# Kernel optimization log

Hardware: AMD Instinct MI355X
Metric: run time of the kernel (lower is better)

Reference implementation:

```python
import jax, jax.numpy as jnp
import numpy as np

K = 32        # top-k per row (init kwarg k)
TAU = 1.0     # gumbel temperature (init kwarg tau)
EPS = 1e-08
NEG_INF = -1e9


def setup_inputs() -> dict:
    key = jax.random.key(0)
    k1, k2 = jax.random.split(key)
    N = 8192
    logits = jax.random.normal(k1, (N, N), dtype=jnp.float32)
    u = jax.random.uniform(k2, (N, N), dtype=jnp.float32)
    return {"logits": logits, "u": u}


def reference(logits, u):
    # Gumbel noise: -log(-log(U + eps) + eps), matching torch.rand_like usage
    gumbel = -jnp.log(-jnp.log(u + EPS) + EPS)
    perturbed = (logits + gumbel) / TAU
    # Row-wise top-k indices on perturbed logits
    _, top_idx = jax.lax.top_k(perturbed, K)          # [N, K]
    # Scatter a hard 0/1 mask at the selected indices
    N = logits.shape[0]
    rows = jnp.arange(N)[:, None]                      # [N, 1]
    mask = jnp.zeros_like(logits).at[rows, top_idx].set(1.0)
    # Masked softmax over the ORIGINAL logits (noise only selects)
    masked_logits = logits * mask + (1.0 - mask) * NEG_INF
    adjacency = jax.nn.softmax(masked_logits, axis=-1)
    return adjacency
```

## Files before the change

### kernel.cpp

```cpp
#include <hip/hip_runtime.h>
#include <cstdint>

#define ROW_N 8192
#define TPB   256
#define CAP   512

__device__ __forceinline__ unsigned int fkey(float p) {
  unsigned int b = __float_as_uint(p);
  return (b & 0x80000000u) ? ~b : (b | 0x80000000u);
}
__device__ __forceinline__ float fkey_inv(unsigned int t) {
  unsigned int b = (t & 0x80000000u) ? (t & 0x7fffffffu) : ~t;
  return __uint_as_float(b);
}

__device__ __forceinline__ unsigned int akey(float lg, float uu) {
  float l2u = __log2f(uu + 1e-8f);
  float w   = fmaf(l2u, -0.6931471805599453f, 1e-8f);
  float p2  = fmaf(lg, 1.4426950408889634f, -__log2f(w));
  p2 = (w < 1e-5f) ? 3.0e38f : p2;
  return fkey(p2);
}

__device__ __forceinline__ uint64_t shfl_xor_u64(uint64_t v, int m) {
  unsigned int lo = (unsigned int)v, hi = (unsigned int)(v >> 32);
  lo = __shfl_xor(lo, m, 64);
  hi = __shfl_xor(hi, m, 64);
  return ((uint64_t)hi << 32) | lo;
}
__device__ __forceinline__ uint64_t wave_max_u64(uint64_t v) {
#pragma unroll
  for (int s = 32; s >= 1; s >>= 1) {
    uint64_t o = shfl_xor_u64(v, s);
    v = (o > v) ? o : v;
  }
  return v;
}

__global__ __launch_bounds__(TPB) void gumbel_topk_kernel(
    const float* __restrict__ logits, const float* __restrict__ u,
    float* __restrict__ out) {
  const int row  = blockIdx.x;
  const int tid  = threadIdx.x;
  const int lane = tid & 63;
  const int wave = tid >> 6;

  __shared__ unsigned int s_cnt, s_t;
  __shared__ unsigned int s_tmax[TPB];
  __shared__ unsigned int s_idx[CAP];
  __shared__ uint64_t     s_comp[CAP];
  __shared__ float        s_lg[CAP];
  __shared__ float        s_red[8];

  if (tid == 0) { s_cnt = 0; s_t = 0xFFFFFFFFu; }

  const float4* L4 = reinterpret_cast<const float4*>(logits) + (size_t)row * (ROW_N / 4);
  const float4* U4 = reinterpret_cast<const float4*>(u)      + (size_t)row * (ROW_N / 4);
  float4*       O4 = reinterpret_cast<float4*>(out)          + (size_t)row * (ROW_N / 4);

  unsigned int k[32];
  unsigned int M = 0;
#pragma unroll
  for (int j = 0; j < 8; ++j) {
    float4 lv = L4[j * TPB + tid];
    float4 uv = U4[j * TPB + tid];
    k[j * 4 + 0] = akey(lv.x, uv.x);
    k[j * 4 + 1] = akey(lv.y, uv.y);
    k[j * 4 + 2] = akey(lv.z, uv.z);
    k[j * 4 + 3] = akey(lv.w, uv.w);
    M = max(M, max(max(k[j * 4 + 0], k[j * 4 + 1]), max(k[j * 4 + 2], k[j * 4 + 3])));
  }

  {
    float4 z = make_float4(0.f, 0.f, 0.f, 0.f);
#pragma unroll
    for (int j = 0; j < 8; ++j) O4[j * TPB + tid] = z;
  }

  s_tmax[tid] = M;
  __syncthreads();
  {
    unsigned int cnt = 0;
    const uint4* tm4 = reinterpret_cast<const uint4*>(s_tmax);
#pragma unroll 4
    for (int i = 0; i < TPB / 4; ++i) {
      uint4 v = tm4[i];
      cnt += (v.x > M) + (v.y > M) + (v.z > M) + (v.w > M);
    }
    if (cnt < 32) atomicMin(&s_t, M);
  }
  __syncthreads();
  const unsigned int tm = fkey(fkey_inv(s_t) - 0.25f);

#pragma unroll
  for (int j = 0; j < 8; ++j) {
#pragma unroll
    for (int c = 0; c < 4; ++c) {
      if (k[j * 4 + c] >= tm) {
        unsigned int slot = atomicAdd(&s_cnt, 1u);
        if (slot < CAP)
          s_idx[slot] = (unsigned int)(j * TPB + tid) * 4u + (unsigned int)c;
      }
    }
  }
  __syncthreads();
  unsigned int C = s_cnt;

  if (C > CAP) {
#pragma unroll 1
    for (int it = 0; it < 32; ++it) {
      uint64_t lm = 0;
#pragma unroll
      for (int i = 0; i < 32; ++i) {
        unsigned int idx = (unsigned int)((i >> 2) * TPB + tid) * 4u + (unsigned int)(i & 3);
        uint64_t comp = ((uint64_t)k[i] << 13) | (uint64_t)(8191u - idx);
        if (k[i] != 0u && comp > lm) lm = comp;
      }
      uint64_t wm = wave_max_u64(lm);
      if (lm == wm) {
#pragma unroll
        for (int i = 0; i < 32; ++i) {
          unsigned int idx = (unsigned int)((i >> 2) * TPB + tid) * 4u + (unsigned int)(i & 3);
          uint64_t comp = ((uint64_t)k[i] << 13) | (uint64_t)(8191u - idx);
          if (comp == wm) k[i] = 0u;
        }
      }
      if (lane == 0) s_idx[wave * 32 + it] = 8191u - (unsigned int)(wm & 8191u);
    }
    __syncthreads();
    C = 128;
  }

  const float* Lrow = logits + (size_t)row * ROW_N;
  const float* Urow = u      + (size_t)row * ROW_N;
#pragma unroll 1
  for (unsigned int vi = tid; vi < C; vi += TPB) {
    unsigned int idx = s_idx[vi];
    float lg = Lrow[idx];
    float uu = Urow[idx];
    float p  = lg - logf(-logf(uu + 1e-8f) + 1e-8f);
    s_comp[vi] = ((uint64_t)fkey(p) << 13) | (uint64_t)(8191u - idx);
    s_lg[vi]   = lg;
  }
  __syncthreads();

  float m_local = -3.4e38f;
  unsigned int sel = 0;
  float lgs[2];
  unsigned int ids[2];
#pragma unroll
  for (int s = 0; s < 2; ++s) {
    unsigned int vi = tid + s * TPB;
    lgs[s] = 0.f; ids[s] = 0;
    if (vi < C) {
      uint64_t mine = s_comp[vi];
      unsigned int cnt = 0;
#pragma unroll 1
      for (unsigned int i = 0; i < C; ++i) cnt += (s_comp[i] > mine) ? 1u : 0u;
      if (cnt < 32) {
        sel |= (1u << s);
        lgs[s] = s_lg[vi];
        ids[s] = s_idx[vi];
        m_local = fmaxf(m_local, lgs[s]);
      }
    }
  }

  float m = m_local;
#pragma unroll
  for (int s = 32; s >= 1; s >>= 1) m = fmaxf(m, __shfl_xor(m, s, 64));
  if (lane == 0) s_red[wave] = m;
  __syncthreads();
  m = fmaxf(fmaxf(s_red[0], s_red[1]), fmaxf(s_red[2], s_red[3]));

  float e0 = (sel & 1u) ? expf(lgs[0] - m) : 0.f;
  float e1 = (sel & 2u) ? expf(lgs[1] - m) : 0.f;
  float sum = e0 + e1;
#pragma unroll
  for (int s = 32; s >= 1; s >>= 1) sum += __shfl_xor(sum, s, 64);
  if (lane == 0) s_red[4 + wave] = sum;
  __syncthreads();
  sum = (s_red[4] + s_red[5]) + (s_red[6] + s_red[7]);

  float* Orow = out + (size_t)row * ROW_N;
  if (sel & 1u) Orow[ids[0]] = e0 / sum;
  if (sel & 2u) Orow[ids[1]] = e1 / sum;
}

extern "C" void kernel_launch(void* const* d_in, const int* in_sizes, int n_in,
                              void* d_out, int out_size, void* d_ws, size_t ws_size,
                              hipStream_t stream) {
  const float* logits = (const float*)d_in[0];
  const float* u      = (const float*)d_in[1];
  float*       out    = (float*)d_out;
  int rows = in_sizes[0] / ROW_N;
  gumbel_topk_kernel<<<dim3(rows), dim3(TPB), 0, stream>>>(logits, u, out);
}
```

Baseline: 618.2 us.

## Use 1024-thread blocks with wave-level second-max threshold and saturated-key handling

Raises the block size from 256 to 1024 threads, so each thread holds 8 keys instead of 32. The per-thread count over a shared max array is replaced by two wave max reductions that find each wave's second-largest thread max; the minimum across 16 waves becomes the candidate threshold. Saturated Gumbel values now get a lower-bound key and are always admitted as candidates instead of being forced to infinity. This lowers register pressure and the serial work per thread, in exchange for more waves per block, more candidates in the final pairwise ranking, and extra sync cost.

```diff
diff --git a/kernel.cpp b/kernel.cpp
--- a/kernel.cpp
+++ b/kernel.cpp
@@ -2,8 +2,10 @@
 #include <cstdint>
 
 #define ROW_N 8192
-#define TPB   256
-#define CAP   512
+#define TPB   1024
+#define NW    16
+#define EPT   8
+#define CAP   1024
 
 __device__ __forceinline__ unsigned int fkey(float p) {
   unsigned int b = __float_as_uint(p);
@@ -14,12 +16,13 @@
   return __uint_as_float(b);
 }
 
-__device__ __forceinline__ unsigned int akey(float lg, float uu) {
+__device__ __forceinline__ unsigned int akey(float lg, float uu, bool& sat) {
   float l2u = __log2f(uu + 1e-8f);
   float w   = fmaf(l2u, -0.6931471805599453f, 1e-8f);
+  sat = (w < 1e-5f);
   float p2  = fmaf(lg, 1.4426950408889634f, -__log2f(w));
-  p2 = (w < 1e-5f) ? 3.0e38f : p2;
-  return fkey(p2);
+  float lb  = (lg + 11.512925f) * 1.4426950408889634f;
+  return fkey(sat ? lb : p2);
 }
 
 __device__ __forceinline__ uint64_t shfl_xor_u64(uint64_t v, int m) {
@@ -36,8 +39,16 @@
   }
   return v;
 }
+__device__ __forceinline__ unsigned int wave_max_u32(unsigned int v) {
+#pragma unroll
+  for (int s = 32; s >= 1; s >>= 1) {
+    unsigned int o = __shfl_xor(v, s, 64);
+    v = max(v, o);
+  }
+  return v;
+}
 
-__global__ __launch_bounds__(TPB) void gumbel_topk_kernel(
+__global__ __launch_bounds__(TPB, 8) void gumbel_topk_kernel(
     const float* __restrict__ logits, const float* __restrict__ u,
     float* __restrict__ out) {
   const int row  = blockIdx.x;
@@ -45,62 +56,58 @@
   const int lane = tid & 63;
   const int wave = tid >> 6;
 
-  __shared__ unsigned int s_cnt, s_t;
-  __shared__ unsigned int s_tmax[TPB];
+  __shared__ unsigned int s_cnt;
+  __shared__ unsigned int s_tw[NW];
   __shared__ unsigned int s_idx[CAP];
   __shared__ uint64_t     s_comp[CAP];
   __shared__ float        s_lg[CAP];
-  __shared__ float        s_red[8];
+  __shared__ float        s_red[NW];
+  __shared__ float        s_red2[NW];
 
-  if (tid == 0) { s_cnt = 0; s_t = 0xFFFFFFFFu; }
+  if (tid == 0) s_cnt = 0;
 
   const float4* L4 = reinterpret_cast<const float4*>(logits) + (size_t)row * (ROW_N / 4);
   const float4* U4 = reinterpret_cast<const float4*>(u)      + (size_t)row * (ROW_N / 4);
   float4*       O4 = reinterpret_cast<float4*>(out)          + (size_t)row * (ROW_N / 4);
 
-  unsigned int k[32];
+  unsigned int k[EPT];
+  unsigned int satm = 0;
   unsigned int M = 0;
 #pragma unroll
-  for (int j = 0; j < 8; ++j) {
+  for (int j = 0; j < EPT / 4; ++j) {
     float4 lv = L4[j * TPB + tid];
     float4 uv = U4[j * TPB + tid];
-    k[j * 4 + 0] = akey(lv.x, uv.x);
-    k[j * 4 + 1] = akey(lv.y, uv.y);
-    k[j * 4 + 2] = akey(lv.z, uv.z);
-    k[j * 4 + 3] = akey(lv.w, uv.w);
+    bool s0, s1, s2, s3;
+    k[j * 4 + 0] = akey(lv.x, uv.x, s0);
+    k[j * 4 + 1] = akey(lv.y, uv.y, s1);
+    k[j * 4 + 2] = akey(lv.z, uv.z, s2);
+    k[j * 4 + 3] = akey(lv.w, uv.w, s3);
+    satm |= ((s0 ? 1u : 0u) | (s1 ? 2u : 0u) | (s2 ? 4u : 0u) | (s3 ? 8u : 0u)) << (j * 4);
     M = max(M, max(max(k[j * 4 + 0], k[j * 4 + 1]), max(k[j * 4 + 2], k[j * 4 + 3])));
   }
 
   {
     float4 z = make_float4(0.f, 0.f, 0.f, 0.f);
 #pragma unroll
-    for (int j = 0; j < 8; ++j) O4[j * TPB + tid] = z;
+    for (int j = 0; j < EPT / 4; ++j) O4[j * TPB + tid] = z;
   }
 
-  s_tmax[tid] = M;
+  unsigned int wm1 = wave_max_u32(M);
+  unsigned int Mx  = (M == wm1) ? 0u : M;
+  unsigned int wm2 = wave_max_u32(Mx);
+  if (lane == 0) s_tw[wave] = wm2;
   __syncthreads();
-  {
-    unsigned int cnt = 0;
-    const uint4* tm4 = reinterpret_cast<const uint4*>(s_tmax);
-#pragma unroll 4
-    for (int i = 0; i < TPB / 4; ++i) {
-      uint4 v = tm4[i];
-      cnt += (v.x > M) + (v.y > M) + (v.z > M) + (v.w > M);
-    }
-    if (cnt < 32) atomicMin(&s_t, M);
-  }
-  __syncthreads();
-  const unsigned int tm = fkey(fkey_inv(s_t) - 0.25f);
+  unsigned int t = 0xFFFFFFFFu;
+#pragma unroll
+  for (int i = 0; i < NW; ++i) t = min(t, s_tw[i]);
+  unsigned int tm = (t == 0u) ? 0u : fkey(fkey_inv(t) - 0.25f);
 
 #pragma unroll
-  for (int j = 0; j < 8; ++j) {
-#pragma unroll
-    for (int c = 0; c < 4; ++c) {
-      if (k[j * 4 + c] >= tm) {
-        unsigned int slot = atomicAdd(&s_cnt, 1u);
-        if (slot < CAP)
-          s_idx[slot] = (unsigned int)(j * TPB + tid) * 4u + (unsigned int)c;
-      }
+  for (int i = 0; i < EPT; ++i) {
+    if (k[i] >= tm || ((satm >> i) & 1u)) {
+      unsigned int slot = atomicAdd(&s_cnt, 1u);
+      if (slot < CAP)
+        s_idx[slot] = (unsigned int)((i >> 2) * (TPB * 4) + tid * 4 + (i & 3));
     }
   }
   __syncthreads();
@@ -111,16 +118,16 @@
     for (int it = 0; it < 32; ++it) {
       uint64_t lm = 0;
 #pragma unroll
-      for (int i = 0; i < 32; ++i) {
-        unsigned int idx = (unsigned int)((i >> 2) * TPB + tid) * 4u + (unsigned int)(i & 3);
+      for (int i = 0; i < EPT; ++i) {
+        unsigned int idx = (unsigned int)((i >> 2) * (TPB * 4) + tid * 4 + (i & 3));
         uint64_t comp = ((uint64_t)k[i] << 13) | (uint64_t)(8191u - idx);
         if (k[i] != 0u && comp > lm) lm = comp;
       }
       uint64_t wm = wave_max_u64(lm);
-      if (lm == wm) {
+      if (lm == wm && lm != 0) {
 #pragma unroll
-        for (int i = 0; i < 32; ++i) {
-          unsigned int idx = (unsigned int)((i >> 2) * TPB + tid) * 4u + (unsigned int)(i & 3);
+        for (int i = 0; i < EPT; ++i) {
+          unsigned int idx = (unsigned int)((i >> 2) * (TPB * 4) + tid * 4 + (i & 3));
           uint64_t comp = ((uint64_t)k[i] << 13) | (uint64_t)(8191u - idx);
           if (comp == wm) k[i] = 0u;
         }
@@ -128,63 +135,52 @@
       if (lane == 0) s_idx[wave * 32 + it] = 8191u - (unsigned int)(wm & 8191u);
     }
     __syncthreads();
-    C = 128;
+    C = NW * 32;
   }
 
   const float* Lrow = logits + (size_t)row * ROW_N;
   const float* Urow = u      + (size_t)row * ROW_N;
-#pragma unroll 1
-  for (unsigned int vi = tid; vi < C; vi += TPB) {
-    unsigned int idx = s_idx[vi];
-    float lg = Lrow[idx];
+  float lg = 0.f;
+  unsigned int idx = 0;
+  if (tid < (int)C) {
+    idx = s_idx[tid];
+    lg  = Lrow[idx];
     float uu = Urow[idx];
     float p  = lg - logf(-logf(uu + 1e-8f) + 1e-8f);
-    s_comp[vi] = ((uint64_t)fkey(p) << 13) | (uint64_t)(8191u - idx);
-    s_lg[vi]   = lg;
+    s_comp[tid] = ((uint64_t)fkey(p) << 13) | (uint64_t)(8191u - idx);
+    s_lg[tid]   = lg;
   }
   __syncthreads();
 
-  float m_local = -3.4e38f;
-  unsigned int sel = 0;
-  float lgs[2];
-  unsigned int ids[2];
-#pragma unroll
-  for (int s = 0; s < 2; ++s) {
-    unsigned int vi = tid + s * TPB;
-    lgs[s] = 0.f; ids[s] = 0;
-    if (vi < C) {
-      uint64_t mine = s_comp[vi];
-      unsigned int cnt = 0;
+  bool sel = false;
+  if (tid < (int)C) {
+    uint64_t mine = s_comp[tid];
+    unsigned int cnt = 0;
 #pragma unroll 1
-      for (unsigned int i = 0; i < C; ++i) cnt += (s_comp[i] > mine) ? 1u : 0u;
-      if (cnt < 32) {
-        sel |= (1u << s);
-        lgs[s] = s_lg[vi];
-        ids[s] = s_idx[vi];
-        m_local = fmaxf(m_local, lgs[s]);
-      }
-    }
+    for (unsigned int i = 0; i < C; ++i) cnt += (s_comp[i] > mine) ? 1u : 0u;
+    sel = (cnt < 32);
   }
 
-  float m = m_local;
+  float mv = sel ? lg : -3.4e38f;
 #pragma unroll
-  for (int s = 32; s >= 1; s >>= 1) m = fmaxf(m, __shfl_xor(m, s, 64));
-  if (lane == 0) s_red[wave] = m;
+  for (int s = 32; s >= 1; s >>= 1) mv = fmaxf(mv, __shfl_xor(mv, s, 64));
+  if (lane == 0) s_red[wave] = mv;
   __syncthreads();
-  m = fmaxf(fmaxf(s_red[0], s_red[1]), fmaxf(s_red[2], s_red[3]));
+  float m = -3.4e38f;
+#pragma unroll
+  for (int i = 0; i < NW; ++i) m = fmaxf(m, s_red[i]);
 
-  float e0 = (sel & 1u) ? expf(lgs[0] - m) : 0.f;
-  float e1 = (sel & 2u) ? expf(lgs[1] - m) : 0.f;
-  float sum = e0 + e1;
+  float e = sel ? __expf(lg - m) * 0.f + expf(lg - m) : 0.f;
+  float sum = e;
 #pragma unroll
   for (int s = 32; s >= 1; s >>= 1) sum += __shfl_xor(sum, s, 64);
-  if (lane == 0) s_red[4 + wave] = sum;
+  if (lane == 0) s_red2[wave] = sum;
   __syncthreads();
-  sum = (s_red[4] + s_red[5]) + (s_red[6] + s_red[7]);
+  sum = 0.f;
+#pragma unroll
+  for (int i = 0; i < NW; ++i) sum += s_red2[i];
 
-  float* Orow = out + (size_t)row * ROW_N;
-  if (sel & 1u) Orow[ids[0]] = e0 / sum;
-  if (sel & 2u) Orow[ids[1]] = e1 / sum;
+  if (sel) out[(size_t)row * ROW_N + idx] = e / sum;
 }
 
 extern "C" void kernel_launch(void* const* d_in, const int* in_sizes, int n_in,
```

After: 626.1 us. About the same (+1.3%).
